# Performance work log

Hardware: AMD Instinct MI355X
Metric: run time of the kernel (lower is better)

## Reference

```python
import jax, jax.numpy as jnp
import numpy as np

NUM_HEADS = 16
NUM_FEATURES = 256
EPSILON = 1e-4


def _gaussian_orthogonal_matrix(num_rows, num_cols, seed=0):
    # Stacked transposed-Q blocks from QR of Gaussian blocks, scaled by sqrt(num_cols)
    rng = np.random.default_rng(seed)
    blocks = []
    for _ in range(num_rows // num_cols):
        a = rng.standard_normal((num_cols, num_cols))
        qm, _ = np.linalg.qr(a)
        blocks.append(qm.T)
    rem = num_rows - (num_rows // num_cols) * num_cols
    if rem > 0:
        a = rng.standard_normal((num_cols, num_cols))
        qm, _ = np.linalg.qr(a)
        blocks.append(qm.T[:rem])
    mat = np.concatenate(blocks, axis=0) * np.sqrt(num_cols)
    return jnp.asarray(mat, dtype=jnp.float32)


def setup_inputs() -> dict:
    key = jax.random.key(0)
    kq, kk, kv = jax.random.split(key, 3)
    B, L, D = 4, 4096, 1024
    q = jax.random.normal(kq, (B, L, D), dtype=jnp.float32)
    k = jax.random.normal(kk, (B, L, D), dtype=jnp.float32)
    v = jax.random.normal(kv, (B, L, D), dtype=jnp.float32)
    W = _gaussian_orthogonal_matrix(NUM_FEATURES, D // NUM_HEADS)
    return {"q": q, "k": k, "v": v, "W": W}


def _split_heads(x, H):
    B, L, D = x.shape
    return x.reshape(B, L, H, D // H).transpose(0, 2, 1, 3)  # [B,H,L,d]


def _phi(x, W, is_query, eps):
    # x: [B,H,L,d], W: [m,d]
    h = -0.5 * jnp.sum(x * x, axis=-1, keepdims=True)          # [B,H,L,1]
    proj = jnp.einsum('bhld,md->bhlm', x, W)                   # [B,H,L,m]
    # For queries, max over last dim of h (size-1) == h itself; for keys, global max.
    stab = h if is_query else jnp.max(h)
    ker = jnp.exp(h + proj - stab)
    m = W.shape[0]
    return (m ** -0.5) * (ker + eps)


def reference(q, k, v, W):
    H = NUM_HEADS
    eps = EPSILON
    B, L, D = q.shape
    scale = D ** -0.25  # note: uses full model dim, as in the original code
    qh = _split_heads(q, H) * scale
    kh = _split_heads(k, H) * scale
    vh = _split_heads(v, H)
    q_prime = _phi(qh, W, True, eps)   # [B,H,L,m]
    k_prime = _phi(kh, W, False, eps)  # [B,H,L,m]
    # denominator: q' @ sum_l k'
    d_ = jnp.einsum('bhlm,bhm->bhl', q_prime, jnp.sum(k_prime, axis=-2))[..., None]
    d_ = d_ + 2.0 * eps * (jnp.abs(d_) <= eps).astype(d_.dtype)
    kv = jnp.einsum('bhlm,bhld->bhmd', k_prime, vh)            # [B,H,m,d]
    out = jnp.einsum('bhlm,bhmd->bhld', q_prime, kv) / d_      # [B,H,L,d]
    return out.transpose(0, 2, 1, 3).reshape(B, L, D)
```

## Files before the change

### kernel.cpp

```cpp
#include <hip/hip_runtime.h>


typedef unsigned short u16;
typedef __attribute__((ext_vector_type(8))) short s8v;
typedef __attribute__((ext_vector_type(4))) float f4v;

#define NB 4
#define NL 4096
#define ND 1024
#define NH 16
#define HDIM 64
#define NM 256

#define SCALE 0.17677669529663687f
#define RSQM 0.0625f
#define FEPS 1e-4f
#define ECLAMP 80.0f

#define MFMA16(a, b, c) __builtin_amdgcn_mfma_f32_16x16x32_bf16((a), (b), (c), 0, 0, 0)

__device__ __forceinline__ u16 f2bf(float x) {
  unsigned u = __float_as_uint(x);
  u += 0x7FFFu + ((u >> 16) & 1u);
  return (u16)(u >> 16);
}
__device__ __forceinline__ float bf2f(u16 b) {
  return __uint_as_float(((unsigned)b) << 16);
}

__device__ __forceinline__ void mk2(const float4& a, const float4& b, float sc,
                                    s8v& hi, s8v& lo, float& ss) {
  float f[8] = {a.x * sc, a.y * sc, a.z * sc, a.w * sc,
                b.x * sc, b.y * sc, b.z * sc, b.w * sc};
#pragma unroll
  for (int e = 0; e < 8; e++) {
    ss = fmaf(f[e], f[e], ss);
    u16 h = f2bf(f[e]);
    u16 l = f2bf(f[e] - bf2f(h));
    hi[e] = (short)h;
    lo[e] = (short)l;
  }
}

__global__ void prep_kernel(const float* __restrict__ wp, u16* __restrict__ WfH,
                            u16* __restrict__ WfL, float* __restrict__ kvx) {
  const int idx = blockIdx.x * 512 + threadIdx.x;
  const int e = idx & 7, ln = (idx >> 3) & 63, mt = (idx >> 9) & 15, kk = idx >> 13;
  const int m = mt * 16 + (ln & 15);
  const int d = kk * 32 + ((ln >> 4) << 3) + e;
  const float x = wp[m * HDIM + d];
  const u16 hh = f2bf(x);
  WfH[idx] = hh;
  WfL[idx] = f2bf(x - bf2f(hh));
  for (int i = idx; i < 64 * 256 * 80; i += 16384) kvx[i] = 0.f;
}

__global__ __launch_bounds__(512, 4) void kv_kernel(
    const float* __restrict__ kg, const float* __restrict__ vg,
    const u16* __restrict__ WfH, const u16* __restrict__ WfL,
    float* __restrict__ kvx) {
  const int bh = blockIdx.x >> 3, ch = blockIdx.x & 7;
  const int b = bh >> 4, h = bh & 15;
  const int tid = threadIdx.x, lane = tid & 63, w = tid >> 6;
  const int l15 = lane & 15, g = lane >> 4;

  __shared__ __align__(16) u16 kpH[256][40];
  __shared__ __align__(16) u16 kpL[256][40];
  __shared__ __align__(16) float Vl[32][72];

  const int rt = w & 1, mg = w >> 1;
  const int mtb = 2 * w;

  f4v zero4 = {0.f, 0.f, 0.f, 0.f};
  f4v acc[2][5];
#pragma unroll
  for (int i = 0; i < 2; i++)
#pragma unroll
    for (int j = 0; j < 5; j++) acc[i][j] = zero4;

  s8v oneh = {0, 0, 0, 0, 0, 0, 0, 0};
  if (l15 == 0) {
#pragma unroll
    for (int e = 0; e < 8; e++) oneh[e] = (short)0x3F80;
  }

  const int svr = tid >> 4, svc = (tid & 15) * 4;

  for (int it = 0; it < 16; it++) {
    const int rbase = ch * 512 + it * 32;
    const float4 vv =
        *(const float4*)(vg + (size_t)(b * NL + rbase + svr) * ND + h * HDIM + svc);
    const float* kb = kg + (size_t)(b * NL + rbase + rt * 16 + l15) * ND + h * HDIM;
    const float4 ka0 = *(const float4*)(kb + g * 8);
    const float4 ka1 = *(const float4*)(kb + g * 8 + 4);
    const float4 ka2 = *(const float4*)(kb + 32 + g * 8);
    const float4 ka3 = *(const float4*)(kb + 32 + g * 8 + 4);
    s8v a0h, a0l, a1h, a1l;
    float ss = 0.f;
    mk2(ka0, ka1, SCALE, a0h, a0l, ss);
    mk2(ka2, ka3, SCALE, a1h, a1l, ss);
    ss += __shfl_xor(ss, 16);
    ss += __shfl_xor(ss, 32);
    const float cneg = -0.5f * ss;

    int itz = it;
    asm volatile("" : "+v"(itz));
    const u16* WfHp = WfH + (itz & 0x7FFF0000);
    const u16* WfLp = WfL + (itz & 0x7FFF0000);

    u16 hs[4][4], ls[4][4];
#pragma unroll
    for (int mi = 0; mi < 4; mi++) {
      const int mt = mg * 4 + mi;
      const s8v b0h = *(const s8v*)(WfHp + (size_t)(mt * 64 + lane) * 8);
      const s8v b0l = *(const s8v*)(WfLp + (size_t)(mt * 64 + lane) * 8);
      const s8v b1h = *(const s8v*)(WfHp + (size_t)((16 + mt) * 64 + lane) * 8);
      const s8v b1l = *(const s8v*)(WfLp + (size_t)((16 + mt) * 64 + lane) * 8);
      f4v p = zero4;
      p = MFMA16(a0h, b0h, p);
      p = MFMA16(a1h, b1h, p);
      p = MFMA16(a0h, b0l, p);
      p = MFMA16(a1h, b1l, p);
      p = MFMA16(a0l, b0h, p);
      p = MFMA16(a1l, b1h, p);
#pragma unroll
      for (int r = 0; r < 4; r++) {
        const float cc = __shfl(cneg, 4 * g + r);
        const float arg = fminf(p[r] + cc, ECLAMP);
        const float kv_ = RSQM * __expf(arg) + (RSQM * FEPS);
        const u16 hh = f2bf(kv_);
        hs[mi][r] = hh;
        ls[mi][r] = f2bf(kv_ - bf2f(hh));
      }
    }
    __syncthreads();
#pragma unroll
    for (int mi = 0; mi < 4; mi++) {
      const int m = (mg * 4 + mi) * 16 + l15;
      *(ushort4*)&kpH[m][rt * 16 + 4 * g] =
          make_ushort4(hs[mi][0], hs[mi][1], hs[mi][2], hs[mi][3]);
      *(ushort4*)&kpL[m][rt * 16 + 4 * g] =
          make_ushort4(ls[mi][0], ls[mi][1], ls[mi][2], ls[mi][3]);
    }
    *(float4*)&Vl[svr][svc] = vv;
    __syncthreads();

    const s8v A0h = *(const s8v*)&kpH[mtb * 16 + l15][8 * g];
    const s8v A0l = *(const s8v*)&kpL[mtb * 16 + l15][8 * g];
    const s8v A1h = *(const s8v*)&kpH[(mtb + 1) * 16 + l15][8 * g];
    const s8v A1l = *(const s8v*)&kpL[(mtb + 1) * 16 + l15][8 * g];
#pragma unroll
    for (int ct = 0; ct < 4; ct++) {
      s8v vh, vl;
#pragma unroll
      for (int e = 0; e < 8; e++) {
        const float x = Vl[8 * g + e][ct * 16 + l15];
        const u16 hh = f2bf(x);
        vh[e] = (short)hh;
        vl[e] = (short)f2bf(x - bf2f(hh));
      }
      acc[0][ct] = MFMA16(A0h, vh, acc[0][ct]);
      acc[0][ct] = MFMA16(A0h, vl, acc[0][ct]);
      acc[0][ct] = MFMA16(A0l, vh, acc[0][ct]);
      acc[1][ct] = MFMA16(A1h, vh, acc[1][ct]);
      acc[1][ct] = MFMA16(A1h, vl, acc[1][ct]);
      acc[1][ct] = MFMA16(A1l, vh, acc[1][ct]);
    }
    acc[0][4] = MFMA16(A0h, oneh, acc[0][4]);
    acc[0][4] = MFMA16(A0l, oneh, acc[0][4]);
    acc[1][4] = MFMA16(A1h, oneh, acc[1][4]);
    acc[1][4] = MFMA16(A1l, oneh, acc[1][4]);
  }

  float* kvb = kvx + (size_t)bh * (256 * 80);
#pragma unroll
  for (int mi = 0; mi < 2; mi++)
#pragma unroll
    for (int ct = 0; ct < 5; ct++)
#pragma unroll
      for (int r = 0; r < 4; r++) {
        const int m = (mtb + mi) * 16 + 4 * g + r;
        const int c = ct * 16 + l15;
        atomicAdd(&kvb[m * 80 + c], acc[mi][ct][r]);
      }
}

__global__ __launch_bounds__(512) void fragk_kernel(const float* __restrict__ kvx,
                                                    u16* __restrict__ kvfH,
                                                    u16* __restrict__ kvfL) {
  const int bh = blockIdx.x;
  const float* kb = kvx + (size_t)bh * (256 * 80);
  for (int f = threadIdx.x; f < 20480; f += 512) {
    const int kk = f / 2560;
    const int r1 = f - kk * 2560;
    const int ct = r1 >> 9;
    const int r2 = r1 & 511;
    const int ln = r2 >> 3, e = r2 & 7;
    const int m = kk * 32 + ((ln >> 4) << 3) + e;
    const int c = ct * 16 + (ln & 15);
    const float x = kb[m * 80 + c];
    const u16 hh = f2bf(x);
    kvfH[(size_t)bh * 20480 + f] = hh;
    kvfL[(size_t)bh * 20480 + f] = f2bf(x - bf2f(hh));
  }
}

__global__ __launch_bounds__(512, 4) void out_kernel(
    const float* __restrict__ qg, const u16* __restrict__ WfH,
    const u16* __restrict__ WfL, const u16* __restrict__ kvfH,
    const u16* __restrict__ kvfL, float* __restrict__ outp) {
  const int bh = blockIdx.x >> 6, lt = blockIdx.x & 63;
  const int b = bh >> 4, h = bh & 15;
  const int tid = threadIdx.x, lane = tid & 63, w = tid >> 6;
  const int l15 = lane & 15, g = lane >> 4;

  __shared__ __align__(16) u16 qpH[64][264];
  __shared__ __align__(16) u16 qpL[64][264];
  __shared__ float dinv[64];

  const int rt = w & 3, mh = w >> 2;

  {
    const float* qb = qg + (size_t)(b * NL + lt * 64 + rt * 16 + l15) * ND + h * HDIM;
    const float4 qa0 = *(const float4*)(qb + g * 8);
    const float4 qa1 = *(const float4*)(qb + g * 8 + 4);
    const float4 qa2 = *(const float4*)(qb + 32 + g * 8);
    const float4 qa3 = *(const float4*)(qb + 32 + g * 8 + 4);
    s8v a0h, a0l, a1h, a1l;
    float ss = 0.f;
    mk2(qa0, qa1, SCALE, a0h, a0l, ss);
    mk2(qa2, qa3, SCALE, a1h, a1l, ss);
    f4v zero4 = {0.f, 0.f, 0.f, 0.f};
#pragma unroll
    for (int mi = 0; mi < 8; mi++) {
      const int mt = mh * 8 + mi;
      const s8v b0h = *(const s8v*)(WfH + (size_t)(mt * 64 + lane) * 8);
      const s8v b0l = *(const s8v*)(WfL + (size_t)(mt * 64 + lane) * 8);
      const s8v b1h = *(const s8v*)(WfH + (size_t)((16 + mt) * 64 + lane) * 8);
      const s8v b1l = *(const s8v*)(WfL + (size_t)((16 + mt) * 64 + lane) * 8);
      f4v p = zero4;
      p = MFMA16(a0h, b0h, p);
      p = MFMA16(a1h, b1h, p);
      p = MFMA16(a0h, b0l, p);
      p = MFMA16(a1h, b1l, p);
      p = MFMA16(a0l, b0h, p);
      p = MFMA16(a1l, b1h, p);
#pragma unroll
      for (int r = 0; r < 4; r++) {
        const float arg = fminf(p[r], ECLAMP);
        const float qv = RSQM * __expf(arg) + (RSQM * FEPS);
        const u16 hh = f2bf(qv);
        qpH[rt * 16 + 4 * g + r][mt * 16 + l15] = hh;
        qpL[rt * 16 + 4 * g + r][mt * 16 + l15] = f2bf(qv - bf2f(hh));
      }
    }
  }
  __syncthreads();

  const int ctA = (w < 4) ? 0 : 2;
  const int ctB = ctA + 1;
  f4v o0 = {0.f, 0.f, 0.f, 0.f}, o1 = o0, o2 = o0;
  const size_t fb = (size_t)bh * (8 * 5 * 512);
#pragma unroll
  for (int kk = 0; kk < 8; kk++) {
    const s8v A2h = *(const s8v*)&qpH[rt * 16 + l15][kk * 32 + 8 * g];
    const s8v A2l = *(const s8v*)&qpL[rt * 16 + l15][kk * 32 + 8 * g];
    const size_t bA = fb + (size_t)((kk * 5 + ctA) * 64 + lane) * 8;
    const s8v BAh = *(const s8v*)(kvfH + bA);
    const s8v BAl = *(const s8v*)(kvfL + bA);
    o0 = MFMA16(A2h, BAh, o0);
    o0 = MFMA16(A2h, BAl, o0);
    o0 = MFMA16(A2l, BAh, o0);
    const size_t bB = fb + (size_t)((kk * 5 + ctB) * 64 + lane) * 8;
    const s8v BBh = *(const s8v*)(kvfH + bB);
    const s8v BBl = *(const s8v*)(kvfL + bB);
    o1 = MFMA16(A2h, BBh, o1);
    o1 = MFMA16(A2h, BBl, o1);
    o1 = MFMA16(A2l, BBh, o1);
    if (w < 4) {
      const size_t bC = fb + (size_t)((kk * 5 + 4) * 64 + lane) * 8;
      const s8v BCh = *(const s8v*)(kvfH + bC);
      const s8v BCl = *(const s8v*)(kvfL + bC);
      o2 = MFMA16(A2h, BCh, o2);
      o2 = MFMA16(A2h, BCl, o2);
      o2 = MFMA16(A2l, BCh, o2);
    }
  }
  if (w < 4 && l15 == 0) {
#pragma unroll
    for (int r = 0; r < 4; r++) {
      float d = o2[r];
      if (fabsf(d) <= FEPS) d += 2.0f * FEPS;
      dinv[rt * 16 + 4 * g + r] = 1.0f / d;
    }
  }
  __syncthreads();
  {
    float* ob = outp + (size_t)(b * NL + lt * 64) * ND + h * HDIM;
#pragma unroll
    for (int r = 0; r < 4; r++) {
      const int row = rt * 16 + 4 * g + r;
      const float di = dinv[row];
      ob[(size_t)row * ND + ctA * 16 + l15] = o0[r] * di;
      ob[(size_t)row * ND + ctB * 16 + l15] = o1[r] * di;
    }
  }
}

extern "C" void kernel_launch(void* const* d_in, const int* in_sizes, int n_in,
                              void* d_out, int out_size, void* d_ws, size_t ws_size,
                              hipStream_t stream) {
  const float* q = (const float*)d_in[0];
  const float* k = (const float*)d_in[1];
  const float* v = (const float*)d_in[2];
  const float* w = (const float*)d_in[3];
  float* out = (float*)d_out;

  u16* WfH = (u16*)d_ws;
  u16* WfL = WfH + 16384;
  float* kvx = (float*)((char*)d_ws + 65536);
  u16* kvfH = (u16*)((char*)d_ws + 65536 + (size_t)64 * 256 * 80 * 4);
  u16* kvfL = kvfH + (size_t)64 * 20480;

  prep_kernel<<<32, 512, 0, stream>>>(w, WfH, WfL, kvx);
  kv_kernel<<<512, 512, 0, stream>>>(k, v, WfH, WfL, kvx);
  fragk_kernel<<<64, 512, 0, stream>>>(kvx, kvfH, kvfL);
  out_kernel<<<4096, 512, 0, stream>>>(q, WfH, WfL, kvfH, kvfL, out);
}
```

Before: 422.7 us.

## Pre-split V into bf16 hi/lo fragments once and truncate instead of round

V is now loaded directly in MFMA fragment layout, and each wave converts its slice to either the bf16 hi or lo part once, storing ready fragments in shared memory. This replaces the per-wave redundant conversion of the full V tile from an fp32 shared buffer. The bf16 split also switches from round-to-nearest to truncation, which removes several integer ops per value, and the row-norm shuffles are hoisted out of the m-tile loop. V loads become strided scalar reads instead of float4, and truncated hi parts carry slightly larger residuals, though the lo term still compensates.

```diff
diff --git a/kernel.cpp b/kernel.cpp
--- a/kernel.cpp
+++ b/kernel.cpp
@@ -27,18 +27,22 @@
 __device__ __forceinline__ float bf2f(u16 b) {
   return __uint_as_float(((unsigned)b) << 16);
 }
-
-__device__ __forceinline__ void mk2(const float4& a, const float4& b, float sc,
-                                    s8v& hi, s8v& lo, float& ss) {
+__device__ __forceinline__ u16 bhi(float x) {
+  return (u16)(__float_as_uint(x) >> 16);
+}
+__device__ __forceinline__ float bhif(float x) {
+  return __uint_as_float(__float_as_uint(x) & 0xFFFF0000u);
+}
+
+__device__ __forceinline__ void mk2t(const float4& a, const float4& b, float sc,
+                                     s8v& hi, s8v& lo, float& ss) {
   float f[8] = {a.x * sc, a.y * sc, a.z * sc, a.w * sc,
                 b.x * sc, b.y * sc, b.z * sc, b.w * sc};
 #pragma unroll
   for (int e = 0; e < 8; e++) {
     ss = fmaf(f[e], f[e], ss);
-    u16 h = f2bf(f[e]);
-    u16 l = f2bf(f[e] - bf2f(h));
-    hi[e] = (short)h;
-    lo[e] = (short)l;
+    hi[e] = (short)bhi(f[e]);
+    lo[e] = (short)bhi(f[e] - bhif(f[e]));
   }
 }
 
@@ -66,10 +70,12 @@
 
   __shared__ __align__(16) u16 kpH[256][40];
   __shared__ __align__(16) u16 kpL[256][40];
-  __shared__ __align__(16) float Vl[32][72];
+  __shared__ __align__(16) u16 VfH[4][64][8];
+  __shared__ __align__(16) u16 VfL[4][64][8];
 
   const int rt = w & 1, mg = w >> 1;
   const int mtb = 2 * w;
+  const int vct = w & 3, vhl = w >> 2;
 
   f4v zero4 = {0.f, 0.f, 0.f, 0.f};
   f4v acc[2][5];
@@ -84,12 +90,13 @@
     for (int e = 0; e < 8; e++) oneh[e] = (short)0x3F80;
   }
 
-  const int svr = tid >> 4, svc = (tid & 15) * 4;
-
   for (int it = 0; it < 16; it++) {
     const int rbase = ch * 512 + it * 32;
-    const float4 vv =
-        *(const float4*)(vg + (size_t)(b * NL + rbase + svr) * ND + h * HDIM + svc);
+    const float* vb =
+        vg + (size_t)(b * NL + rbase + 8 * g) * ND + h * HDIM + vct * 16 + l15;
+    float vx[8];
+#pragma unroll
+    for (int e = 0; e < 8; e++) vx[e] = vb[(size_t)e * ND];
     const float* kb = kg + (size_t)(b * NL + rbase + rt * 16 + l15) * ND + h * HDIM;
     const float4 ka0 = *(const float4*)(kb + g * 8);
     const float4 ka1 = *(const float4*)(kb + g * 8 + 4);
@@ -97,11 +104,23 @@
     const float4 ka3 = *(const float4*)(kb + 32 + g * 8 + 4);
     s8v a0h, a0l, a1h, a1l;
     float ss = 0.f;
-    mk2(ka0, ka1, SCALE, a0h, a0l, ss);
-    mk2(ka2, ka3, SCALE, a1h, a1l, ss);
+    mk2t(ka0, ka1, SCALE, a0h, a0l, ss);
+    mk2t(ka2, ka3, SCALE, a1h, a1l, ss);
     ss += __shfl_xor(ss, 16);
     ss += __shfl_xor(ss, 32);
     const float cneg = -0.5f * ss;
+    float ccr[4];
+#pragma unroll
+    for (int r = 0; r < 4; r++) ccr[r] = __shfl(cneg, 4 * g + r);
+
+    s8v vf;
+    if (vhl == 0) {
+#pragma unroll
+      for (int e = 0; e < 8; e++) vf[e] = (short)bhi(vx[e]);
+    } else {
+#pragma unroll
+      for (int e = 0; e < 8; e++) vf[e] = (short)bhi(vx[e] - bhif(vx[e]));
+    }
 
     int itz = it;
     asm volatile("" : "+v"(itz));
@@ -125,12 +144,10 @@
       p = MFMA16(a1l, b1h, p);
 #pragma unroll
       for (int r = 0; r < 4; r++) {
-        const float cc = __shfl(cneg, 4 * g + r);
-        const float arg = fminf(p[r] + cc, ECLAMP);
+        const float arg = fminf(p[r] + ccr[r], ECLAMP);
         const float kv_ = RSQM * __expf(arg) + (RSQM * FEPS);
-        const u16 hh = f2bf(kv_);
-        hs[mi][r] = hh;
-        ls[mi][r] = f2bf(kv_ - bf2f(hh));
+        hs[mi][r] = bhi(kv_);
+        ls[mi][r] = bhi(kv_ - bhif(kv_));
       }
     }
     __syncthreads();
@@ -142,7 +159,10 @@
       *(ushort4*)&kpL[m][rt * 16 + 4 * g] =
           make_ushort4(ls[mi][0], ls[mi][1], ls[mi][2], ls[mi][3]);
     }
-    *(float4*)&Vl[svr][svc] = vv;
+    {
+      u16(*vdst)[64][8] = vhl ? VfL : VfH;
+      *(s8v*)&vdst[vct][lane][0] = vf;
+    }
     __syncthreads();
 
     const s8v A0h = *(const s8v*)&kpH[mtb * 16 + l15][8 * g];
@@ -151,14 +171,8 @@
     const s8v A1l = *(const s8v*)&kpL[(mtb + 1) * 16 + l15][8 * g];
 #pragma unroll
     for (int ct = 0; ct < 4; ct++) {
-      s8v vh, vl;
-#pragma unroll
-      for (int e = 0; e < 8; e++) {
-        const float x = Vl[8 * g + e][ct * 16 + l15];
-        const u16 hh = f2bf(x);
-        vh[e] = (short)hh;
-        vl[e] = (short)f2bf(x - bf2f(hh));
-      }
+      const s8v vh = *(const s8v*)&VfH[ct][lane][0];
+      const s8v vl = *(const s8v*)&VfL[ct][lane][0];
       acc[0][ct] = MFMA16(A0h, vh, acc[0][ct]);
       acc[0][ct] = MFMA16(A0h, vl, acc[0][ct]);
       acc[0][ct] = MFMA16(A0l, vh, acc[0][ct]);
@@ -228,8 +242,8 @@
     const float4 qa3 = *(const float4*)(qb + 32 + g * 8 + 4);
     s8v a0h, a0l, a1h, a1l;
     float ss = 0.f;
-    mk2(qa0, qa1, SCALE, a0h, a0l, ss);
-    mk2(qa2, qa3, SCALE, a1h, a1l, ss);
+    mk2t(qa0, qa1, SCALE, a0h, a0l, ss);
+    mk2t(qa2, qa3, SCALE, a1h, a1l, ss);
     f4v zero4 = {0.f, 0.f, 0.f, 0.f};
 #pragma unroll
     for (int mi = 0; mi < 8; mi++) {
@@ -249,9 +263,8 @@
       for (int r = 0; r < 4; r++) {
         const float arg = fminf(p[r], ECLAMP);
         const float qv = RSQM * __expf(arg) + (RSQM * FEPS);
-        const u16 hh = f2bf(qv);
-        qpH[rt * 16 + 4 * g + r][mt * 16 + l15] = hh;
-        qpL[rt * 16 + 4 * g + r][mt * 16 + l15] = f2bf(qv - bf2f(hh));
+        qpH[rt * 16 + 4 * g + r][mt * 16 + l15] = bhi(qv);
+        qpL[rt * 16 + 4 * g + r][mt * 16 + l15] = bhi(qv - bhif(qv));
       }
     }
   }
```

Result: faster. 399.0 us (-5.6%).
